# Optimization experiments

Hardware: AMD Instinct MI355X
Metric: run time of the kernel (lower is better)

The kernel has to match this reference:

```python
import jax, jax.numpy as jnp
import numpy as np

B, M, N, E = 64, 100, 6400, 102400   # graphs, nodes/graph, total nodes, edges
H, D, EMB, IMG, NC = 4, 512, 768, 1024, 2
HD = H * D
EPS = 1e-5


def _bn2(x, g, b, m, v):
    # BatchNorm1d eval mode on [B, C]
    return (x - m) / jnp.sqrt(v + EPS) * g + b


def _bn3(x, g, b, m, v):
    # BatchNorm1d eval mode on [B, C, L] -> channel dim is axis 1 (node index)
    return (x - m[None, :, None]) / jnp.sqrt(v + EPS)[None, :, None] * g[None, :, None] + b[None, :, None]


def _gat(feat, src, dst, W, al, ar, bias):
    # DGL GATConv (eval: feat_drop is identity). feat: [N, F_in]
    h = (feat @ W.T).reshape(-1, H, D)                 # [N, H, D]
    el = (h * al[None]).sum(-1)                         # [N, H]
    er = (h * ar[None]).sum(-1)                         # [N, H]
    e = jax.nn.leaky_relu(el[src] + er[dst], negative_slope=0.2)  # [E, H]
    mx = jax.ops.segment_max(e, dst, num_segments=N)
    a = jnp.exp(e - mx[dst])
    s = jax.ops.segment_sum(a, dst, num_segments=N)
    alpha = a / s[dst]                                  # edge softmax over incoming edges
    out = jax.ops.segment_sum(h[src] * alpha[:, :, None], dst, num_segments=N)  # [N, H, D]
    return out + bias.reshape(1, H, D)


def setup_inputs() -> dict:
    key = jax.random.key(0)
    ks = iter(jax.random.split(key, 80))
    n = lambda *s: jax.random.normal(next(ks), s, dtype=jnp.float32)

    def bn(c):
        return (1.0 + 0.1 * n(c), 0.1 * n(c), 0.1 * n(c),
                0.5 + jax.random.uniform(next(ks), (c,), dtype=jnp.float32))

    s = 0.02
    inp = {}
    inp['img_embedding'] = n(B, IMG)
    inp['func_text_embedding'] = n(B, EMB)
    inp['unix_emb'] = n(N, EMB)
    inp['pos_emb'] = jax.random.uniform(next(ks), (N, 4), dtype=jnp.float32)
    inp['src'] = jax.random.randint(next(ks), (E,), 0, N)
    inp['dst'] = jax.random.randint(next(ks), (E,), 0, N)
    inp['gat1_W'] = n(HD, EMB) * s; inp['gat1_al'] = n(H, D) * 0.1; inp['gat1_ar'] = n(H, D) * 0.1; inp['gat1_b'] = jnp.zeros(HD)
    inp['gat2_W'] = n(HD, HD) * s; inp['gat2_al'] = n(H, D) * 0.1; inp['gat2_ar'] = n(H, D) * 0.1; inp['gat2_b'] = jnp.zeros(HD)
    inp['fc_W'] = n(D, HD) * s; inp['fc_b'] = jnp.zeros(D)
    inp['hidden_W'] = n(8, D, D) * s; inp['hidden_b'] = jnp.zeros((8, D))
    inp['bn_text_g'], inp['bn_text_b'], inp['bn_text_m'], inp['bn_text_v'] = bn(EMB)
    inp['fc_text_W'] = n(D, EMB) * s; inp['fc_text_b'] = jnp.zeros(D)
    inp['swin_g'], inp['swin_b'], inp['swin_m'], inp['swin_v'] = bn(IMG)
    inp['swinfc_W'] = n(D, IMG) * s; inp['swinfc_b'] = jnp.zeros(D)
    inp['bngat_g'], inp['bngat_b'], inp['bngat_m'], inp['bngat_v'] = bn(M)
    inp['fc_gat_W'] = n(480, D) * s; inp['fc_gat_b'] = jnp.zeros(480)
    inp['bnbb_g'], inp['bnbb_b'], inp['bnbb_m'], inp['bnbb_v'] = bn(M)
    inp['fc_bbox_W'] = n(32, 4) * s; inp['fc_bbox_b'] = jnp.zeros(32)
    inp['fbn_g'], inp['fbn_b'], inp['fbn_m'], inp['fbn_v'] = bn(3 * D)
    inp['final_W'] = n(NC, 3 * D) * s; inp['final_b'] = jnp.zeros(NC)
    return inp


def reference(img_embedding, func_text_embedding, unix_emb, pos_emb, src, dst,
              gat1_W, gat1_al, gat1_ar, gat1_b, gat2_W, gat2_al, gat2_ar, gat2_b,
              fc_W, fc_b, hidden_W, hidden_b,
              bn_text_g, bn_text_b, bn_text_m, bn_text_v, fc_text_W, fc_text_b,
              swin_g, swin_b, swin_m, swin_v, swinfc_W, swinfc_b,
              bngat_g, bngat_b, bngat_m, bngat_v, fc_gat_W, fc_gat_b,
              bnbb_g, bnbb_b, bnbb_m, bnbb_v, fc_bbox_W, fc_bbox_b,
              fbn_g, fbn_b, fbn_m, fbn_v, final_W, final_b):
    # image branch
    x = jax.nn.elu(_bn2(img_embedding, swin_g, swin_b, swin_m, swin_v) @ swinfc_W.T + swinfc_b)
    # text branch
    ft = jax.nn.elu(_bn2(func_text_embedding, bn_text_g, bn_text_b, bn_text_m, bn_text_v) @ fc_text_W.T + fc_text_b)
    # graph branch: two stacked GATConv layers (dropout is identity in eval)
    h = _gat(unix_emb, src, dst, gat1_W, gat1_al, gat1_ar, gat1_b).reshape(N, HD)
    h = _gat(h, src, dst, gat2_W, gat2_al, gat2_ar, gat2_b).reshape(N, HD)
    h = jax.nn.elu(h @ fc_W.T + fc_b)
    for i in range(8):
        h = jax.nn.elu(h @ hidden_W[i].T + hidden_b[i])
    # unbatch + pad to max_node=100 -> pure reshape (all graphs have exactly M nodes)
    h_i = h.reshape(B, M, D)
    pos_i = pos_emb.reshape(B, M, 4)
    h_i = jax.nn.elu(_bn3(h_i, bngat_g, bngat_b, bngat_m, bngat_v) @ fc_gat_W.T + fc_gat_b)      # [B, M, 480]
    pos_i = jax.nn.elu(_bn3(pos_i, bnbb_g, bnbb_b, bnbb_m, bnbb_v) @ fc_bbox_W.T + fc_bbox_b)    # [B, M, 32]
    h_feature = jnp.concatenate([h_i, pos_i], axis=2).mean(axis=1)                                # [B, 512]
    all_feats = jnp.concatenate([x, h_feature, ft], axis=1)                                       # [B, 1536]
    return _bn2(all_feats, fbn_g, fbn_b, fbn_m, fbn_v) @ final_W.T + final_b
```

## Files before the change

kernel.cpp:

```cpp
#include <hip/hip_runtime.h>
#include <math.h>

#define Bg   64
#define Mg   100
#define Ng   6400
#define Eg   102400
#define Hh   4
#define Dd   512
#define HDd  2048
#define EMBd 768
#define IMGd 1024
#define EPSc 1e-5f

typedef __bf16 bf16x8 __attribute__((ext_vector_type(8)));
typedef float  f32x4  __attribute__((ext_vector_type(4)));

__device__ __forceinline__ float eluf(float x) { return x > 0.f ? x : expm1f(x); }

__device__ __forceinline__ unsigned short f2bf(float x) {
    unsigned int u = __builtin_bit_cast(unsigned int, x);
    u += 0x7FFFu + ((u >> 16) & 1u);
    return (unsigned short)(u >> 16);
}
__device__ __forceinline__ float bf2f(unsigned short s) {
    return __builtin_bit_cast(float, ((unsigned int)s) << 16);
}

__device__ __forceinline__ void gld16(const void* g, void* l) {
    __builtin_amdgcn_global_load_lds(
        (const __attribute__((address_space(1))) void*)g,
        (__attribute__((address_space(3))) void*)l, 16, 0, 0);
}

__global__ __launch_bounds__(256)
void gemm_bf16(const unsigned short* __restrict__ A,
               const unsigned short* __restrict__ W,
               const float* __restrict__ bias, void* __restrict__ C,
               int M, int N, int K, int act, int outbf)
{
    __shared__ __align__(16) unsigned short As[2][128 * 32];
    __shared__ __align__(16) unsigned short Bs[2][128 * 32];
    const int tid  = threadIdx.x;
    const int lane = tid & 63, wid = tid >> 6;
    const int bm = blockIdx.y * 128, bn = blockIdx.x * 128;
    const int wm = (wid >> 1) * 64, wn = (wid & 1) * 64;
    const int lrow = lane >> 2;
    const int lcol = (lane & 3) << 3;

    f32x4 acc[4][4] = {};

    const int ra = wid * 32;
    const unsigned short* gA0 = A + (size_t)(bm + ra + lrow) * K + lcol;
    const unsigned short* gA1 = A + (size_t)(bm + ra + 16 + lrow) * K + lcol;
    int rb0 = bn + ra + lrow;       if (rb0 >= N) rb0 = N - 1;
    int rb1 = bn + ra + 16 + lrow;  if (rb1 >= N) rb1 = N - 1;
    const unsigned short* gB0 = W + (size_t)rb0 * K + lcol;
    const unsigned short* gB1 = W + (size_t)rb1 * K + lcol;

    const int frow = lane & 15;
    const int quad = (lane >> 4) << 3;
    const int nt = K >> 5;

    gld16(gA0, &As[0][ra * 32]);
    gld16(gA1, &As[0][(ra + 16) * 32]);
    gld16(gB0, &Bs[0][ra * 32]);
    gld16(gB1, &Bs[0][(ra + 16) * 32]);
    __syncthreads();

    int cur = 0;
    for (int t = 0; t < nt; ++t) {
        if (t + 1 < nt) {
            const int k0 = (t + 1) << 5;
            const int nb = cur ^ 1;
            gld16(gA0 + k0, &As[nb][ra * 32]);
            gld16(gA1 + k0, &As[nb][(ra + 16) * 32]);
            gld16(gB0 + k0, &Bs[nb][ra * 32]);
            gld16(gB1 + k0, &Bs[nb][(ra + 16) * 32]);
        }
        bf16x8 af[4], bfr[4];
#pragma unroll
        for (int i = 0; i < 4; ++i)
            af[i]  = *(const bf16x8*)&As[cur][(wm + i * 16 + frow) * 32 + quad];
#pragma unroll
        for (int i = 0; i < 4; ++i)
            bfr[i] = *(const bf16x8*)&Bs[cur][(wn + i * 16 + frow) * 32 + quad];
#pragma unroll
        for (int mi = 0; mi < 4; ++mi)
#pragma unroll
            for (int ni = 0; ni < 4; ++ni)
                acc[mi][ni] = __builtin_amdgcn_mfma_f32_16x16x32_bf16(
                    af[mi], bfr[ni], acc[mi][ni], 0, 0, 0);
        __syncthreads();
        cur ^= 1;
    }

    const int crow0 = bm + wm + ((lane >> 4) << 2);
    const int ccol0 = bn + wn + (lane & 15);
#pragma unroll
    for (int mi = 0; mi < 4; ++mi) {
#pragma unroll
        for (int ni = 0; ni < 4; ++ni) {
            int col = ccol0 + ni * 16;
            if (col >= N) continue;
            float bv = bias ? bias[col] : 0.f;
#pragma unroll
            for (int r = 0; r < 4; ++r) {
                int row = crow0 + mi * 16 + r;
                float v = acc[mi][ni][r] + bv;
                if (act) v = eluf(v);
                if (outbf) ((unsigned short*)C)[(size_t)row * N + col] = f2bf(v);
                else       ((float*)C)[(size_t)row * N + col] = v;
            }
        }
    }
}

__global__ __launch_bounds__(256)
void gemm_bf16_t64(const unsigned short* __restrict__ A,
                   const unsigned short* __restrict__ W,
                   const float* __restrict__ bias, void* __restrict__ C,
                   int M, int N, int K, int act, int outbf)
{
    __shared__ __align__(16) unsigned short As[2][64 * 32];
    __shared__ __align__(16) unsigned short Bs[2][64 * 32];
    const int tid  = threadIdx.x;
    const int lane = tid & 63, wid = tid >> 6;
    const int bm = blockIdx.y * 64, bn = blockIdx.x * 64;
    const int wm = (wid >> 1) * 32, wn = (wid & 1) * 32;
    const int lrow = lane >> 2;
    const int lcol = (lane & 3) << 3;

    f32x4 acc[2][2] = {};

    const int ra = wid * 16;
    const unsigned short* gA = A + (size_t)(bm + ra + lrow) * K + lcol;
    int rb = bn + ra + lrow; if (rb >= N) rb = N - 1;
    const unsigned short* gB = W + (size_t)rb * K + lcol;

    const int frow = lane & 15;
    const int quad = (lane >> 4) << 3;
    const int nt = K >> 5;

    gld16(gA, &As[0][ra * 32]);
    gld16(gB, &Bs[0][ra * 32]);
    __syncthreads();

    int cur = 0;
    for (int t = 0; t < nt; ++t) {
        if (t + 1 < nt) {
            const int k0 = (t + 1) << 5;
            const int nb = cur ^ 1;
            gld16(gA + k0, &As[nb][ra * 32]);
            gld16(gB + k0, &Bs[nb][ra * 32]);
        }
        bf16x8 af0 = *(const bf16x8*)&As[cur][(wm + frow) * 32 + quad];
        bf16x8 af1 = *(const bf16x8*)&As[cur][(wm + 16 + frow) * 32 + quad];
        bf16x8 bf0 = *(const bf16x8*)&Bs[cur][(wn + frow) * 32 + quad];
        bf16x8 bf1 = *(const bf16x8*)&Bs[cur][(wn + 16 + frow) * 32 + quad];
        acc[0][0] = __builtin_amdgcn_mfma_f32_16x16x32_bf16(af0, bf0, acc[0][0], 0, 0, 0);
        acc[0][1] = __builtin_amdgcn_mfma_f32_16x16x32_bf16(af0, bf1, acc[0][1], 0, 0, 0);
        acc[1][0] = __builtin_amdgcn_mfma_f32_16x16x32_bf16(af1, bf0, acc[1][0], 0, 0, 0);
        acc[1][1] = __builtin_amdgcn_mfma_f32_16x16x32_bf16(af1, bf1, acc[1][1], 0, 0, 0);
        __syncthreads();
        cur ^= 1;
    }

    const int crow0 = bm + wm + ((lane >> 4) << 2);
    const int ccol0 = bn + wn + (lane & 15);
#pragma unroll
    for (int mi = 0; mi < 2; ++mi) {
#pragma unroll
        for (int ni = 0; ni < 2; ++ni) {
            int col = ccol0 + ni * 16;
            if (col >= N) continue;
            float bv = bias ? bias[col] : 0.f;
#pragma unroll
            for (int r = 0; r < 4; ++r) {
                int row = crow0 + mi * 16 + r;
                float v = acc[mi][ni][r] + bv;
                if (act) v = eluf(v);
                if (outbf) ((unsigned short*)C)[(size_t)row * N + col] = f2bf(v);
                else       ((float*)C)[(size_t)row * N + col] = v;
            }
        }
    }
}

__global__ __launch_bounds__(256)
void gemm_nt(const float* __restrict__ A, const float* __restrict__ W,
             const float* __restrict__ bias, float* __restrict__ C,
             int M, int N, int K, int act)
{
    __shared__ float As[16 * 68];
    __shared__ float Ws[16 * 68];
    const int tid = threadIdx.x;
    const int tx = tid & 15, ty = tid >> 4;
    const int bm = blockIdx.y * 64, bn = blockIdx.x * 64;
    const int lrow = tid >> 2;
    const int lk4  = (tid & 3) << 2;
    const int arow = bm + lrow;
    const int wrow = bn + lrow;
    const float* Aptr = A + (size_t)arow * K + lk4;
    const float* Wptr = W + (size_t)wrow * K + lk4;
    float acc[4][4] = {{0.f,0.f,0.f,0.f},{0.f,0.f,0.f,0.f},{0.f,0.f,0.f,0.f},{0.f,0.f,0.f,0.f}};

    for (int k0 = 0; k0 < K; k0 += 16) {
        float4 av = make_float4(0.f,0.f,0.f,0.f);
        float4 wv = make_float4(0.f,0.f,0.f,0.f);
        if (arow < M) av = *(const float4*)(Aptr + k0);
        if (wrow < N) wv = *(const float4*)(Wptr + k0);
        As[(lk4+0)*68 + lrow] = av.x;
        As[(lk4+1)*68 + lrow] = av.y;
        As[(lk4+2)*68 + lrow] = av.z;
        As[(lk4+3)*68 + lrow] = av.w;
        Ws[(lk4+0)*68 + lrow] = wv.x;
        Ws[(lk4+1)*68 + lrow] = wv.y;
        Ws[(lk4+2)*68 + lrow] = wv.z;
        Ws[(lk4+3)*68 + lrow] = wv.w;
        __syncthreads();
#pragma unroll
        for (int kk = 0; kk < 16; ++kk) {
            float4 a = *(const float4*)&As[kk*68 + (ty<<2)];
            float4 w = *(const float4*)&Ws[kk*68 + (tx<<2)];
            acc[0][0] += a.x*w.x; acc[0][1] += a.x*w.y; acc[0][2] += a.x*w.z; acc[0][3] += a.x*w.w;
            acc[1][0] += a.y*w.x; acc[1][1] += a.y*w.y; acc[1][2] += a.y*w.z; acc[1][3] += a.y*w.w;
            acc[2][0] += a.z*w.x; acc[2][1] += a.z*w.y; acc[2][2] += a.z*w.z; acc[2][3] += a.z*w.w;
            acc[3][0] += a.w*w.x; acc[3][1] += a.w*w.y; acc[3][2] += a.w*w.z; acc[3][3] += a.w*w.w;
        }
        __syncthreads();
    }

#pragma unroll
    for (int i = 0; i < 4; ++i) {
        int row = bm + (ty<<2) + i;
        int col = bn + (tx<<2);
        if (row < M && col < N) {
            float4 v;
            v.x = acc[i][0]; v.y = acc[i][1]; v.z = acc[i][2]; v.w = acc[i][3];
            if (bias) { v.x += bias[col]; v.y += bias[col+1]; v.z += bias[col+2]; v.w += bias[col+3]; }
            if (act == 1) { v.x = eluf(v.x); v.y = eluf(v.y); v.z = eluf(v.z); v.w = eluf(v.w); }
            *(float4*)(C + (size_t)row * N + col) = v;
        }
    }
}

struct CvtPack {
    const float* s[6];
    unsigned short* d[6];
    int n4[6];
};

__global__ void cvt_all(CvtPack p, int total4)
{
    int i = blockIdx.x * 256 + threadIdx.x;
    if (i >= total4) return;
#pragma unroll
    for (int k = 0; k < 6; ++k) {
        if (i < p.n4[k]) {
            float4 v = ((const float4*)p.s[k])[i];
            ushort4 o;
            o.x = f2bf(v.x); o.y = f2bf(v.y); o.z = f2bf(v.z); o.w = f2bf(v.w);
            ((ushort4*)p.d[k])[i] = o;
            return;
        }
        i -= p.n4[k];
    }
}

__global__ void bn_col(const float* __restrict__ x, const float* __restrict__ g,
                       const float* __restrict__ b, const float* __restrict__ m,
                       const float* __restrict__ v, float* __restrict__ y,
                       int rows, int cols)
{
    int i = blockIdx.x * 256 + threadIdx.x;
    if (i >= rows * cols) return;
    int c = i % cols;
    float inv = rsqrtf(v[c] + EPSc);
    y[i] = (x[i] - m[c]) * inv * g[c] + b[c];
}

__global__ void bn_node_b4(const ushort4* __restrict__ x, const float* __restrict__ g,
                           const float* __restrict__ b, const float* __restrict__ m,
                           const float* __restrict__ v, ushort4* __restrict__ y,
                           int total4, int Cdim4)
{
    int i = blockIdx.x * 256 + threadIdx.x;
    if (i >= total4) return;
    int n = i / Cdim4;
    int p = n % Mg;
    float sc = rsqrtf(v[p] + EPSc) * g[p];
    float sh = b[p] - m[p] * sc;
    ushort4 xv = x[i];
    ushort4 o;
    o.x = f2bf(bf2f(xv.x) * sc + sh);
    o.y = f2bf(bf2f(xv.y) * sc + sh);
    o.z = f2bf(bf2f(xv.z) * sc + sh);
    o.w = f2bf(bf2f(xv.w) * sc + sh);
    y[i] = o;
}

__global__ void zero_i32(int* __restrict__ p, int n)
{
    int i = blockIdx.x * 256 + threadIdx.x;
    if (i < n) p[i] = 0;
}

__global__ void count_dst(const int* __restrict__ dst, int* __restrict__ counts, int E)
{
    int i = blockIdx.x * 256 + threadIdx.x;
    if (i < E) atomicAdd(&counts[dst[i]], 1);
}

__global__ __launch_bounds__(1024)
void scan_excl(const int* __restrict__ counts, int* __restrict__ offs,
               int* __restrict__ cursor, int n)
{
    __shared__ int sm[1024];
    __shared__ int carry;
    if (threadIdx.x == 0) carry = 0;
    __syncthreads();
    for (int base = 0; base < n; base += 1024) {
        int i = base + (int)threadIdx.x;
        int v = (i < n) ? counts[i] : 0;
        sm[threadIdx.x] = v;
        __syncthreads();
        for (int o = 1; o < 1024; o <<= 1) {
            int t = (threadIdx.x >= (unsigned)o) ? sm[threadIdx.x - o] : 0;
            __syncthreads();
            sm[threadIdx.x] += t;
            __syncthreads();
        }
        int incl = sm[threadIdx.x];
        int myc = carry;
        if (i < n) {
            int ex = myc + incl - v;
            offs[i] = ex;
            cursor[i] = ex;
        }
        __syncthreads();
        if (threadIdx.x == 1023) carry = myc + sm[1023];
        __syncthreads();
    }
    if (threadIdx.x == 0) offs[n] = carry;
}

__global__ void scatter_edges(const int* __restrict__ dst, int* __restrict__ cursor,
                              int* __restrict__ eid, int E)
{
    int i = blockIdx.x * 256 + threadIdx.x;
    if (i < E) {
        int p = atomicAdd(&cursor[dst[i]], 1);
        eid[p] = i;
    }
}

__global__ __launch_bounds__(256)
void elr_kernel(const unsigned short* __restrict__ Hm, const float* __restrict__ al,
                const float* __restrict__ ar, float* __restrict__ el,
                float* __restrict__ er)
{
    int wid = threadIdx.x >> 6, lane = threadIdx.x & 63;
    int g = (blockIdx.x << 2) + wid;
    int n = g >> 2, h = g & 3;
    const unsigned short* hp = Hm + ((size_t)n << 11) + (h << 9) + (lane << 3);
    const float* alp = al + (h << 9) + (lane << 3);
    const float* arp = ar + (h << 9) + (lane << 3);
    ushort4 x0 = *(const ushort4*)hp;
    ushort4 x1 = *(const ushort4*)(hp + 4);
    float4 l0 = *(const float4*)alp, l1 = *(const float4*)(alp + 4);
    float4 r0 = *(const float4*)arp, r1 = *(const float4*)(arp + 4);
    float a0 = bf2f(x0.x), a1 = bf2f(x0.y), a2 = bf2f(x0.z), a3 = bf2f(x0.w);
    float a4 = bf2f(x1.x), a5 = bf2f(x1.y), a6 = bf2f(x1.z), a7 = bf2f(x1.w);
    float se = a0*l0.x + a1*l0.y + a2*l0.z + a3*l0.w + a4*l1.x + a5*l1.y + a6*l1.z + a7*l1.w;
    float sr = a0*r0.x + a1*r0.y + a2*r0.z + a3*r0.w + a4*r1.x + a5*r1.y + a6*r1.z + a7*r1.w;
#pragma unroll
    for (int o = 32; o > 0; o >>= 1) {
        se += __shfl_down(se, o, 64);
        sr += __shfl_down(sr, o, 64);
    }
    if (lane == 0) { el[g] = se; er[g] = sr; }
}

__global__ __launch_bounds__(256)
void gat_agg(const unsigned short* __restrict__ Hm, const float* __restrict__ el,
             const float* __restrict__ er, const int* __restrict__ src,
             const int* __restrict__ offs, const int* __restrict__ eid,
             const float* __restrict__ bias, unsigned short* __restrict__ out)
{
    int n = blockIdx.x;
    int tid = threadIdx.x;
    int beg = offs[n], end = offs[n + 1];
    int deg = end - beg;
    const int b0 = tid << 2;
    const int b1 = 1024 + (tid << 2);
    const int h0 = tid >> 7;
    const int h1 = h0 + 2;

    if (deg == 0) {
#pragma unroll
        for (int j = 0; j < 4; ++j) {
            out[((size_t)n << 11) + b0 + j] = f2bf(bias[b0 + j]);
            out[((size_t)n << 11) + b1 + j] = f2bf(bias[b1 + j]);
        }
        return;
    }

    __shared__ float m_sh[4], s_sh[4], al_sh[4];
    __shared__ int   src_sh[128];
    __shared__ float logit_sh[512];
    __shared__ float w_sh[512];

    if (tid < 4) { m_sh[tid] = -INFINITY; s_sh[tid] = 0.f; }
    float acc[8] = {0.f,0.f,0.f,0.f,0.f,0.f,0.f,0.f};
    __syncthreads();

    for (int c0 = 0; c0 < deg; c0 += 128) {
        int cnt = min(128, deg - c0);
        for (int i = tid; i < cnt; i += 256) src_sh[i] = src[eid[beg + c0 + i]];
        __syncthreads();
        for (int idx = tid; idx < (cnt << 2); idx += 256) {
            int i = idx >> 2, h = idx & 3;
            float x = el[(src_sh[i] << 2) + h] + er[(n << 2) + h];
            logit_sh[idx] = x > 0.f ? x : 0.2f * x;
        }
        __syncthreads();
        if (tid < 4) {
            float cm = -INFINITY;
            for (int i = 0; i < cnt; ++i) cm = fmaxf(cm, logit_sh[(i << 2) + tid]);
            float mn = fmaxf(m_sh[tid], cm);
            al_sh[tid] = expf(m_sh[tid] - mn);
            m_sh[tid] = mn;
        }
        __syncthreads();
        for (int idx = tid; idx < (cnt << 2); idx += 256)
            w_sh[idx] = expf(logit_sh[idx] - m_sh[idx & 3]);
        __syncthreads();
        if (tid < 4) {
            float cs = 0.f;
            for (int i = 0; i < cnt; ++i) cs += w_sh[(i << 2) + tid];
            s_sh[tid] = s_sh[tid] * al_sh[tid] + cs;
        }
        float r0 = al_sh[h0], r1 = al_sh[h1];
        acc[0] *= r0; acc[1] *= r0; acc[2] *= r0; acc[3] *= r0;
        acc[4] *= r1; acc[5] *= r1; acc[6] *= r1; acc[7] *= r1;
        for (int i = 0; i < cnt; ++i) {
            const unsigned short* hp = Hm + ((size_t)src_sh[i] << 11);
            ushort4 a = *(const ushort4*)(hp + b0);
            ushort4 b = *(const ushort4*)(hp + b1);
            float w0 = w_sh[(i << 2) + h0], w1 = w_sh[(i << 2) + h1];
            acc[0] += w0 * bf2f(a.x); acc[1] += w0 * bf2f(a.y);
            acc[2] += w0 * bf2f(a.z); acc[3] += w0 * bf2f(a.w);
            acc[4] += w1 * bf2f(b.x); acc[5] += w1 * bf2f(b.y);
            acc[6] += w1 * bf2f(b.z); acc[7] += w1 * bf2f(b.w);
        }
        __syncthreads();
    }

    float is0 = 1.f / s_sh[h0], is1 = 1.f / s_sh[h1];
#pragma unroll
    for (int j = 0; j < 4; ++j) {
        out[((size_t)n << 11) + b0 + j] = f2bf(acc[j] * is0 + bias[b0 + j]);
        out[((size_t)n << 11) + b1 + j] = f2bf(acc[4 + j] * is1 + bias[b1 + j]);
    }
}

__global__ void mean_kernel(const float* __restrict__ hg, const float* __restrict__ pos,
                            const float* __restrict__ bg, const float* __restrict__ bb_,
                            const float* __restrict__ bm_, const float* __restrict__ bv_,
                            const float* __restrict__ W, const float* __restrict__ bias,
                            float* __restrict__ hf)
{
    int i = blockIdx.x * 256 + threadIdx.x;
    if (i >= Bg * Dd) return;
    int bb = i >> 9, c = i & 511;
    float s = 0.f;
    if (c < 480) {
        const float* p = hg + (size_t)bb * Mg * 480 + c;
        for (int mm = 0; mm < Mg; ++mm) s += p[mm * 480];
    } else {
        int o = c - 480;
        float w0 = W[(o << 2) + 0], w1 = W[(o << 2) + 1];
        float w2 = W[(o << 2) + 2], w3 = W[(o << 2) + 3];
        float bo = bias[o];
        const float* pp = pos + (size_t)bb * Mg * 4;
        for (int mm = 0; mm < Mg; ++mm) {
            float sc = rsqrtf(bv_[mm] + EPSc) * bg[mm];
            float sh = bb_[mm] - bm_[mm] * sc;
            float a = bo + (pp[mm*4+0]*sc+sh)*w0 + (pp[mm*4+1]*sc+sh)*w1
                         + (pp[mm*4+2]*sc+sh)*w2 + (pp[mm*4+3]*sc+sh)*w3;
            s += eluf(a);
        }
    }
    hf[i] = s * 0.01f;
}

__global__ __launch_bounds__(256)
void final_kernel(const float* __restrict__ x, const float* __restrict__ hf,
                  const float* __restrict__ ft, const float* __restrict__ g,
                  const float* __restrict__ b, const float* __restrict__ m,
                  const float* __restrict__ v, const float* __restrict__ W,
                  const float* __restrict__ bias, float* __restrict__ out)
{
    int bb = blockIdx.x;
    int tid = threadIdx.x;
    float a0 = 0.f, a1 = 0.f;
    for (int c = tid; c < 1536; c += 256) {
        float xv = (c < 512) ? x[bb * 512 + c]
                 : (c < 1024) ? hf[bb * 512 + (c - 512)]
                              : ft[bb * 512 + (c - 1024)];
        float z = (xv - m[c]) * rsqrtf(v[c] + EPSc) * g[c] + b[c];
        a0 += z * W[c];
        a1 += z * W[1536 + c];
    }
    __shared__ float r0[256], r1[256];
    r0[tid] = a0; r1[tid] = a1;
    __syncthreads();
    for (int o = 128; o > 0; o >>= 1) {
        if (tid < o) { r0[tid] += r0[tid + o]; r1[tid] += r1[tid + o]; }
        __syncthreads();
    }
    if (tid == 0) {
        out[bb * 2 + 0] = r0[0] + bias[0];
        out[bb * 2 + 1] = r1[0] + bias[1];
    }
}

extern "C" void kernel_launch(void* const* d_in, const int* in_sizes, int n_in,
                              void* d_out, int out_size, void* d_ws, size_t ws_size,
                              hipStream_t stream)
{
    (void)in_sizes; (void)n_in; (void)out_size; (void)ws_size;

    const float* img   = (const float*)d_in[0];
    const float* ftxt  = (const float*)d_in[1];
    const float* unixe = (const float*)d_in[2];
    const float* pos   = (const float*)d_in[3];
    const int*   src   = (const int*)  d_in[4];
    const int*   dst   = (const int*)  d_in[5];
    const float* g1W   = (const float*)d_in[6];
    const float* g1al  = (const float*)d_in[7];
    const float* g1ar  = (const float*)d_in[8];
    const float* g1b   = (const float*)d_in[9];
    const float* g2W   = (const float*)d_in[10];
    const float* g2al  = (const float*)d_in[11];
    const float* g2ar  = (const float*)d_in[12];
    const float* g2b   = (const float*)d_in[13];
    const float* fcW   = (const float*)d_in[14];
    const float* fcb   = (const float*)d_in[15];
    const float* hidW  = (const float*)d_in[16];
    const float* hidb  = (const float*)d_in[17];
    const float* btg   = (const float*)d_in[18];
    const float* btb   = (const float*)d_in[19];
    const float* btm   = (const float*)d_in[20];
    const float* btv   = (const float*)d_in[21];
    const float* ftW   = (const float*)d_in[22];
    const float* ftbi  = (const float*)d_in[23];
    const float* swg   = (const float*)d_in[24];
    const float* swb   = (const float*)d_in[25];
    const float* swm   = (const float*)d_in[26];
    const float* swv   = (const float*)d_in[27];
    const float* swW   = (const float*)d_in[28];
    const float* swbi  = (const float*)d_in[29];
    const float* bgg   = (const float*)d_in[30];
    const float* bgb   = (const float*)d_in[31];
    const float* bgm   = (const float*)d_in[32];
    const float* bgv   = (const float*)d_in[33];
    const float* fgW   = (const float*)d_in[34];
    const float* fgb   = (const float*)d_in[35];
    const float* bbgp  = (const float*)d_in[36];
    const float* bbbp  = (const float*)d_in[37];
    const float* bbmp  = (const float*)d_in[38];
    const float* bbvp  = (const float*)d_in[39];
    const float* fbW   = (const float*)d_in[40];
    const float* fbb   = (const float*)d_in[41];
    const float* fng   = (const float*)d_in[42];
    const float* fnb   = (const float*)d_in[43];
    const float* fnm   = (const float*)d_in[44];
    const float* fnv   = (const float*)d_in[45];
    const float* fiW   = (const float*)d_in[46];
    const float* fib   = (const float*)d_in[47];
    float* out = (float*)d_out;

    char* p = (char*)d_ws;
    unsigned short* fA  = (unsigned short*)p; p += (size_t)Ng * HDd * 2;
    unsigned short* fB  = (unsigned short*)p; p += (size_t)Ng * HDd * 2;
    unsigned short* fC  = (unsigned short*)p; p += (size_t)Ng * Dd * 2;
    unsigned short* fD  = (unsigned short*)p; p += (size_t)Ng * Dd * 2;
    float*          fE  = (float*)p;          p += (size_t)Ng * 480 * 4;
    float*          el  = (float*)p;          p += (size_t)Ng * Hh * 4;
    float*          er  = (float*)p;          p += (size_t)Ng * Hh * 4;
    float*          xb  = (float*)p;          p += (size_t)Bg * Dd * 4;
    float*          ftb = (float*)p;          p += (size_t)Bg * Dd * 4;
    float*          hf  = (float*)p;          p += (size_t)Bg * Dd * 4;
    float*          ti  = (float*)p;          p += (size_t)Bg * IMGd * 4;
    float*          tt  = (float*)p;          p += (size_t)Bg * EMBd * 4;
    unsigned short* ubf = (unsigned short*)p; p += (size_t)Ng * EMBd * 2;
    unsigned short* wg1 = (unsigned short*)p; p += (size_t)HDd * EMBd * 2;
    unsigned short* wg2 = (unsigned short*)p; p += (size_t)HDd * HDd * 2;
    unsigned short* wfc = (unsigned short*)p; p += (size_t)Dd * HDd * 2;
    unsigned short* whid= (unsigned short*)p; p += (size_t)8 * Dd * Dd * 2;
    unsigned short* wfg = (unsigned short*)p; p += (size_t)480 * Dd * 2;
    int* counts = (int*)p; p += (size_t)Ng * 4;
    int* offs   = (int*)p; p += (size_t)(Ng + 1) * 4 + 12;
    int* cursor = (int*)p; p += (size_t)Ng * 4;
    int* eid    = (int*)p; p += (size_t)Eg * 4;

    CvtPack cp;
    cp.s[0] = unixe; cp.d[0] = ubf;  cp.n4[0] = Ng * EMBd / 4;
    cp.s[1] = g1W;   cp.d[1] = wg1;  cp.n4[1] = HDd * EMBd / 4;
    cp.s[2] = g2W;   cp.d[2] = wg2;  cp.n4[2] = HDd * HDd / 4;
    cp.s[3] = fcW;   cp.d[3] = wfc;  cp.n4[3] = Dd * HDd / 4;
    cp.s[4] = hidW;  cp.d[4] = whid; cp.n4[4] = 8 * Dd * Dd / 4;
    cp.s[5] = fgW;   cp.d[5] = wfg;  cp.n4[5] = 480 * Dd / 4;
    int total4 = cp.n4[0] + cp.n4[1] + cp.n4[2] + cp.n4[3] + cp.n4[4] + cp.n4[5];
    cvt_all<<<(total4 + 255)/256, 256, 0, stream>>>(cp, total4);

    bn_col<<<(Bg*IMGd + 255)/256, 256, 0, stream>>>(img, swg, swb, swm, swv, ti, Bg, IMGd);
    gemm_nt<<<dim3(8, 1), 256, 0, stream>>>(ti, swW, swbi, xb, Bg, Dd, IMGd, 1);
    bn_col<<<(Bg*EMBd + 255)/256, 256, 0, stream>>>(ftxt, btg, btb, btm, btv, tt, Bg, EMBd);
    gemm_nt<<<dim3(8, 1), 256, 0, stream>>>(tt, ftW, ftbi, ftb, Bg, Dd, EMBd, 1);

    zero_i32<<<(Ng + 255)/256, 256, 0, stream>>>(counts, Ng);
    count_dst<<<(Eg + 255)/256, 256, 0, stream>>>(dst, counts, Eg);
    scan_excl<<<1, 1024, 0, stream>>>(counts, offs, cursor, Ng);
    scatter_edges<<<(Eg + 255)/256, 256, 0, stream>>>(dst, cursor, eid, Eg);

    gemm_bf16<<<dim3(HDd/128, Ng/128), 256, 0, stream>>>(ubf, wg1, nullptr, fA, Ng, HDd, EMBd, 0, 1);
    elr_kernel<<<Ng, 256, 0, stream>>>(fA, g1al, g1ar, el, er);
    gat_agg<<<Ng, 256, 0, stream>>>(fA, el, er, src, offs, eid, g1b, fB);

    gemm_bf16<<<dim3(HDd/128, Ng/128), 256, 0, stream>>>(fB, wg2, nullptr, fA, Ng, HDd, HDd, 0, 1);
    elr_kernel<<<Ng, 256, 0, stream>>>(fA, g2al, g2ar, el, er);
    gat_agg<<<Ng, 256, 0, stream>>>(fA, el, er, src, offs, eid, g2b, fB);

    gemm_bf16_t64<<<dim3(Dd/64, Ng/64), 256, 0, stream>>>(fB, wfc, fcb, fC, Ng, Dd, HDd, 1, 1);

    unsigned short* cur = fC; unsigned short* nxt = fD;
    for (int i = 0; i < 8; ++i) {
        gemm_bf16_t64<<<dim3(Dd/64, Ng/64), 256, 0, stream>>>(
            cur, whid + (size_t)i * Dd * Dd, hidb + (size_t)i * Dd, nxt, Ng, Dd, Dd, 1, 1);
        unsigned short* t = cur; cur = nxt; nxt = t;
    }

    bn_node_b4<<<(Ng*Dd/4 + 255)/256, 256, 0, stream>>>(
        (const ushort4*)cur, bgg, bgb, bgm, bgv, (ushort4*)nxt, Ng*Dd/4, Dd/4);
    gemm_bf16_t64<<<dim3(8, Ng/64), 256, 0, stream>>>(nxt, wfg, fgb, fE, Ng, 480, Dd, 1, 0);

    mean_kernel<<<(Bg*Dd + 255)/256, 256, 0, stream>>>(fE, pos, bbgp, bbbp, bbmp, bbvp, fbW, fbb, hf);

    final_kernel<<<Bg, 256, 0, stream>>>(xb, hf, ftb, fng, fnb, fnm, fnv, fiW, fib, out);
}
```

Before: 829.9 us.

## Keep two global-to-LDS loads in flight with explicit vmcnt waits in GEMMs

Both bf16 MFMA GEMM kernels now issue the first two K-tiles of global-to-LDS loads up front. Each iteration waits with a partial vmcnt, so the load for tile t+1 stays in flight while tile t is computed. The plain __syncthreads is replaced with explicit s_waitcnt, s_barrier and sched_barrier fences, and the slot just consumed is refilled with tile t+2. The aim is to hide global load latency better than the old issue-one-ahead scheme, at the cost of fragile hand-counted waitcnt values and scheduling barriers that limit compiler reordering.

```diff
diff --git a/kernel.cpp b/kernel.cpp
--- a/kernel.cpp
+++ b/kernel.cpp
@@ -15,6 +15,9 @@
 typedef __bf16 bf16x8 __attribute__((ext_vector_type(8)));
 typedef float  f32x4  __attribute__((ext_vector_type(4)));
 
+#define SBAR __builtin_amdgcn_sched_barrier(0)
+#define WBAR __builtin_amdgcn_s_barrier()
+
 __device__ __forceinline__ float eluf(float x) { return x > 0.f ? x : expm1f(x); }
 
 __device__ __forceinline__ unsigned short f2bf(float x) {
@@ -61,38 +64,45 @@
     const int quad = (lane >> 4) << 3;
     const int nt = K >> 5;
 
-    gld16(gA0, &As[0][ra * 32]);
-    gld16(gA1, &As[0][(ra + 16) * 32]);
-    gld16(gB0, &Bs[0][ra * 32]);
-    gld16(gB1, &Bs[0][(ra + 16) * 32]);
-    __syncthreads();
-
-    int cur = 0;
+#define STAGE128(t, b)                                  \
+    do {                                                \
+        const int k0_ = (t) << 5;                       \
+        gld16(gA0 + k0_, &As[b][ra * 32]);              \
+        gld16(gA1 + k0_, &As[b][(ra + 16) * 32]);       \
+        gld16(gB0 + k0_, &Bs[b][ra * 32]);              \
+        gld16(gB1 + k0_, &Bs[b][(ra + 16) * 32]);       \
+    } while (0)
+
+    STAGE128(0, 0);
+    if (nt > 1) STAGE128(1, 1);
+
     for (int t = 0; t < nt; ++t) {
-        if (t + 1 < nt) {
-            const int k0 = (t + 1) << 5;
-            const int nb = cur ^ 1;
-            gld16(gA0 + k0, &As[nb][ra * 32]);
-            gld16(gA1 + k0, &As[nb][(ra + 16) * 32]);
-            gld16(gB0 + k0, &Bs[nb][ra * 32]);
-            gld16(gB1 + k0, &Bs[nb][(ra + 16) * 32]);
-        }
+        const int bi = t & 1;
+        SBAR;
+        if (t + 1 < nt) { asm volatile("s_waitcnt vmcnt(4)" ::: "memory"); }
+        else            { asm volatile("s_waitcnt vmcnt(0)" ::: "memory"); }
+        SBAR; WBAR; SBAR;
+
         bf16x8 af[4], bfr[4];
 #pragma unroll
         for (int i = 0; i < 4; ++i)
-            af[i]  = *(const bf16x8*)&As[cur][(wm + i * 16 + frow) * 32 + quad];
+            af[i]  = *(const bf16x8*)&As[bi][(wm + i * 16 + frow) * 32 + quad];
 #pragma unroll
         for (int i = 0; i < 4; ++i)
-            bfr[i] = *(const bf16x8*)&Bs[cur][(wn + i * 16 + frow) * 32 + quad];
+            bfr[i] = *(const bf16x8*)&Bs[bi][(wn + i * 16 + frow) * 32 + quad];
 #pragma unroll
         for (int mi = 0; mi < 4; ++mi)
 #pragma unroll
             for (int ni = 0; ni < 4; ++ni)
                 acc[mi][ni] = __builtin_amdgcn_mfma_f32_16x16x32_bf16(
                     af[mi], bfr[ni], acc[mi][ni], 0, 0, 0);
-        __syncthreads();
-        cur ^= 1;
-    }
+
+        SBAR;
+        asm volatile("s_waitcnt lgkmcnt(0)" ::: "memory");
+        SBAR; WBAR; SBAR;
+        if (t + 2 < nt) STAGE128(t + 2, bi);
+    }
+#undef STAGE128
 
     const int crow0 = bm + wm + ((lane >> 4) << 2);
     const int ccol0 = bn + wn + (lane & 15);
@@ -141,29 +151,38 @@
     const int quad = (lane >> 4) << 3;
     const int nt = K >> 5;
 
-    gld16(gA, &As[0][ra * 32]);
-    gld16(gB, &Bs[0][ra * 32]);
-    __syncthreads();
-
-    int cur = 0;
+#define STAGE64(t, b)                           \
+    do {                                        \
+        const int k0_ = (t) << 5;               \
+        gld16(gA + k0_, &As[b][ra * 32]);       \
+        gld16(gB + k0_, &Bs[b][ra * 32]);       \
+    } while (0)
+
+    STAGE64(0, 0);
+    if (nt > 1) STAGE64(1, 1);
+
     for (int t = 0; t < nt; ++t) {
-        if (t + 1 < nt) {
-            const int k0 = (t + 1) << 5;
-            const int nb = cur ^ 1;
-            gld16(gA + k0, &As[nb][ra * 32]);
-            gld16(gB + k0, &Bs[nb][ra * 32]);
-        }
-        bf16x8 af0 = *(const bf16x8*)&As[cur][(wm + frow) * 32 + quad];
-        bf16x8 af1 = *(const bf16x8*)&As[cur][(wm + 16 + frow) * 32 + quad];
-        bf16x8 bf0 = *(const bf16x8*)&Bs[cur][(wn + frow) * 32 + quad];
-        bf16x8 bf1 = *(const bf16x8*)&Bs[cur][(wn + 16 + frow) * 32 + quad];
+        const int bi = t & 1;
+        SBAR;
+        if (t + 1 < nt) { asm volatile("s_waitcnt vmcnt(2)" ::: "memory"); }
+        else            { asm volatile("s_waitcnt vmcnt(0)" ::: "memory"); }
+        SBAR; WBAR; SBAR;
+
+        bf16x8 af0 = *(const bf16x8*)&As[bi][(wm + frow) * 32 + quad];
+        bf16x8 af1 = *(const bf16x8*)&As[bi][(wm + 16 + frow) * 32 + quad];
+        bf16x8 bf0 = *(const bf16x8*)&Bs[bi][(wn + frow) * 32 + quad];
+        bf16x8 bf1 = *(const bf16x8*)&Bs[bi][(wn + 16 + frow) * 32 + quad];
         acc[0][0] = __builtin_amdgcn_mfma_f32_16x16x32_bf16(af0, bf0, acc[0][0], 0, 0, 0);
         acc[0][1] = __builtin_amdgcn_mfma_f32_16x16x32_bf16(af0, bf1, acc[0][1], 0, 0, 0);
         acc[1][0] = __builtin_amdgcn_mfma_f32_16x16x32_bf16(af1, bf0, acc[1][0], 0, 0, 0);
         acc[1][1] = __builtin_amdgcn_mfma_f32_16x16x32_bf16(af1, bf1, acc[1][1], 0, 0, 0);
-        __syncthreads();
-        cur ^= 1;
-    }
+
+        SBAR;
+        asm volatile("s_waitcnt lgkmcnt(0)" ::: "memory");
+        SBAR; WBAR; SBAR;
+        if (t + 2 < nt) STAGE64(t + 2, bi);
+    }
+#undef STAGE64
 
     const int crow0 = bm + wm + ((lane >> 4) << 2);
     const int ccol0 = bn + wn + (lane & 15);
```

Result: no change. 818.9 us (-1.3%).
